# Optimization experiments

Hardware: AMD Instinct MI355X
Metric: run time of the kernel (lower is better)

The kernel has to match this reference:

```python
import jax, jax.numpy as jnp
import numpy as np

# Blade metric for Cl(1,3) inner product <~A B>_0: sign per basis blade =
# (-1)^{k(k-1)/2} * prod(eta_ii) with eta = diag(1,-1,-1,-1).
# Order: 1 | e0 e1 e2 e3 | e01 e02 e03 e12 e13 e23 | e012 e013 e023 e123 | e0123
BLADE_METRIC = jnp.array(
    [1.0,
     1.0, -1.0, -1.0, -1.0,
     1.0, 1.0, 1.0, -1.0, -1.0, -1.0,
     -1.0, -1.0, -1.0, 1.0,
     -1.0],
    dtype=jnp.float32,
)

B, H, N, MVC, SC = 8, 8, 1024, 8, 32


def setup_inputs() -> dict:
    key = jax.random.key(0)
    ks = jax.random.split(key, 6)
    mv_shape = (B, H, N, MVC, 16)
    s_shape = (B, H, N, SC)
    return {
        "q_mv": jax.random.normal(ks[0], mv_shape, dtype=jnp.float32),
        "k_mv": jax.random.normal(ks[1], mv_shape, dtype=jnp.float32),
        "v_mv": jax.random.normal(ks[2], mv_shape, dtype=jnp.float32),
        "q_s": jax.random.normal(ks[3], s_shape, dtype=jnp.float32),
        "k_s": jax.random.normal(ks[4], s_shape, dtype=jnp.float32),
        "v_s": jax.random.normal(ks[5], s_shape, dtype=jnp.float32),
    }


def reference(q_mv, k_mv, v_mv, q_s, k_s, v_s):
    *lead, n_out, mvc, _ = q_mv.shape
    n_in = k_mv.shape[-3]
    sc = q_s.shape[-1]
    d = 16 * mvc + sc  # total feature dim used for the softmax scale

    # Apply GA blade metric to queries, flatten mv channels, concat scalars.
    qf = jnp.concatenate(
        [(q_mv * BLADE_METRIC).reshape(*lead, n_out, mvc * 16), q_s], axis=-1
    )
    kf = jnp.concatenate([k_mv.reshape(*lead, n_in, mvc * 16), k_s], axis=-1)
    vf = jnp.concatenate([v_mv.reshape(*lead, n_in, mvc * 16), v_s], axis=-1)

    scores = jnp.einsum("bhid,bhjd->bhij", qf, kf) / jnp.sqrt(
        jnp.asarray(d, dtype=qf.dtype)
    )
    attn = jax.nn.softmax(scores, axis=-1)
    out = jnp.einsum("bhij,bhjd->bhid", attn, vf)

    out_mv = out[..., : mvc * 16].reshape(*lead, n_out, mvc, 16)
    out_s = out[..., mvc * 16 :]
    return out_mv, out_s
```

## Files before the change

kernel.cpp:

```cpp
#include <hip/hip_runtime.h>

typedef __attribute__((ext_vector_type(8))) _Float16 f16x8;
typedef __attribute__((ext_vector_type(4))) float f32x4;

#define BHn 64
#define Nn 1024

static constexpr int kOutMvElems = 8 * 8 * 1024 * 128;
static constexpr float kScaleLog2e = 0.11405506f;
static constexpr unsigned kNegMask = 0xBF1Cu;
static constexpr int kBlob = 20480;
static constexpr int kPair = 2 * kBlob;

typedef __attribute__((address_space(1))) const void* gas1_t;
typedef __attribute__((address_space(3))) void* las3_t;
__device__ __forceinline__ void dma16(const _Float16* g, _Float16* l) {
  __builtin_amdgcn_global_load_lds((gas1_t)g, (las3_t)l, 16, 0, 0);
}
__device__ __forceinline__ float fast_exp2(float x) {
  float r;
  asm("v_exp_f32 %0, %1" : "=v"(r) : "v"(x));
  return r;
}

__global__ __launch_bounds__(256) void pack_kernel(const float* __restrict__ kmv,
                                                   const float* __restrict__ ks,
                                                   const float* __restrict__ vmv,
                                                   const float* __restrict__ vs,
                                                   _Float16* __restrict__ KV) {
  __shared__ _Float16 tk[64][184];
  __shared__ _Float16 tv[160][72];
  const int kt = blockIdx.x;
  const int bh = blockIdx.y;
  const int tid = threadIdx.x;
#pragma unroll
  for (int i = 0; i < 5; ++i) {
    int s = tid + 256 * i;
    int key = s / 20, p = s - key * 20;
    int row = bh * Nn + kt * 64 + key;
    const float* src = (p < 16) ? (kmv + (size_t)row * 128 + p * 8)
                                : (ks + (size_t)row * 32 + (p - 16) * 8);
    float4 a = *(const float4*)src;
    float4 b = *(const float4*)(src + 4);
    f16x8 h;
    h[0] = (_Float16)a.x; h[1] = (_Float16)a.y; h[2] = (_Float16)a.z; h[3] = (_Float16)a.w;
    h[4] = (_Float16)b.x; h[5] = (_Float16)b.y; h[6] = (_Float16)b.z; h[7] = (_Float16)b.w;
    *(f16x8*)&tk[key][p * 8] = h;
  }
  for (int s = tid; s < 64 * 40; s += 256) {
    int key = s / 40, p = s - key * 40;
    int row = bh * Nn + kt * 64 + key;
    const float* src = (p < 32) ? (vmv + (size_t)row * 128 + p * 4)
                                : (vs + (size_t)row * 32 + (p - 32) * 4);
    float4 v = *(const float4*)src;
    int d = p * 4;
    tv[d + 0][key] = (_Float16)v.x;
    tv[d + 1][key] = (_Float16)v.y;
    tv[d + 2][key] = (_Float16)v.z;
    tv[d + 3][key] = (_Float16)v.w;
  }
  __syncthreads();
  _Float16* dst = KV + ((size_t)bh * 16 + kt) * kBlob;
#pragma unroll
  for (int i = 0; i < 5; ++i) {
    int u = tid + 256 * i;
    int p = u >> 6, key = u & 63;
    f16x8 h = *(const f16x8*)&tk[key][p * 8];
    *(f16x8*)&dst[p * 512 + key * 8] = h;
  }
#pragma unroll
  for (int i = 0; i < 5; ++i) {
    int u = tid + 256 * i;
    int s = u / 160, d = u - s * 160;
    int c32 = (s >> 2) * 32, gg = s & 3;
    f16x8 h;
#pragma unroll
    for (int i2 = 0; i2 < 8; ++i2) {
      int key = c32 + ((i2 < 4) ? (gg * 4 + i2) : (16 + gg * 4 + (i2 - 4)));
      h[i2] = tv[d][key];
    }
    *(f16x8*)&dst[10240 + u * 8] = h;
  }
}

__global__ __launch_bounds__(512, 1) void geo_attn_kernel(const float* __restrict__ qmv,
                                                          const float* __restrict__ qs,
                                                          const _Float16* __restrict__ KV,
                                                          float* __restrict__ out) {
  __shared__ __align__(16) _Float16 kv[2 * kPair];

  const int b = blockIdx.x;
  const int sw = (b & 7) * 32 + (b >> 3);
  const int qb = sw & 3;
  const int bh = sw >> 2;

  const int tid = threadIdx.x;
  const int w = tid >> 6;
  const int l = tid & 63;
  const int g = l >> 4;
  const int nn = l & 15;

  const _Float16* blob0 = KV + (size_t)bh * 16 * kBlob;

  int kbase[5];
#pragma unroll
  for (int c = 0; c < 5; ++c) kbase[c] = (4 * c + g) * 512 + nn * 8;
  int vbase[2];
#pragma unroll
  for (int ch = 0; ch < 2; ++ch) vbase[ch] = 10240 + (4 * ch + g) * 1280 + nn * 8;

  f16x8 qf[2][5];
#pragma unroll
  for (int q2 = 0; q2 < 2; ++q2) {
    const size_t qbase = (size_t)(bh * Nn + qb * 256 + w * 32 + q2 * 16 + nn);
#pragma unroll
    for (int c = 0; c < 5; ++c) {
      const float* src = (c < 4) ? (qmv + qbase * 128 + c * 32 + 8 * g)
                                 : (qs + qbase * 32 + 8 * g);
      float4 a = *(const float4*)src;
      float4 bb = *(const float4*)(src + 4);
      float x[8] = {a.x, a.y, a.z, a.w, bb.x, bb.y, bb.z, bb.w};
#pragma unroll
      for (int i = 0; i < 8; ++i) {
        float v = x[i] * kScaleLog2e;
        if (c < 4) {
          int idx = ((g & 1) << 3) + i;
          v = ((kNegMask >> idx) & 1u) ? -v : v;
        }
        qf[q2][c][i] = (_Float16)v;
      }
    }
  }

  f32x4 acc[2][10];
#pragma unroll
  for (int q2 = 0; q2 < 2; ++q2)
#pragma unroll
    for (int j = 0; j < 10; ++j) acc[q2][j] = (f32x4){0.f, 0.f, 0.f, 0.f};
  float Ma = 12.f, Mb = 12.f, La = 0.f, Lb = 0.f;

  f32x4 sa[4], sb[4];
  f16x8 paf[2], pbf[2];

  const int laneOff = l * 8 + w * 512;
  auto stage = [&](int t, int buf) {
    const _Float16* src = blob0 + (size_t)t * kPair + laneOff;
    _Float16* dst = &kv[buf * kPair + laneOff];
#pragma unroll
    for (int i = 0; i < 10; ++i) dma16(src + i * 4096, dst + i * 4096);
  };

  auto do_qk = [&](const _Float16* blob) {
#pragma unroll
    for (int kb = 0; kb < 4; ++kb) {
      sa[kb] = (f32x4){0.f, 0.f, 0.f, 0.f};
      sb[kb] = (f32x4){0.f, 0.f, 0.f, 0.f};
    }
    f16x8 kf[5][4];
#pragma unroll
    for (int c = 0; c < 2; ++c)
#pragma unroll
      for (int kb = 0; kb < 4; ++kb) kf[c][kb] = *(const f16x8*)&blob[kbase[c] + kb * 128];
#pragma unroll
    for (int c = 0; c < 5; ++c) {
      if (c + 2 < 5) {
#pragma unroll
        for (int kb = 0; kb < 4; ++kb)
          kf[c + 2][kb] = *(const f16x8*)&blob[kbase[c + 2] + kb * 128];
      }
#pragma unroll
      for (int kb = 0; kb < 4; ++kb) {
        sa[kb] = __builtin_amdgcn_mfma_f32_16x16x32_f16(kf[c][kb], qf[0][c], sa[kb], 0, 0, 0);
        sb[kb] = __builtin_amdgcn_mfma_f32_16x16x32_f16(kf[c][kb], qf[1][c], sb[kb], 0, 0, 0);
      }
    }
  };
  auto do_pv = [&](const _Float16* blob) {
    f16x8 vf[20];
#pragma unroll
    for (int i = 0; i < 4; ++i)
      vf[i] = *(const f16x8*)&blob[vbase[i / 10] + (i % 10) * 128];
#pragma unroll
    for (int i = 0; i < 20; ++i) {
      if (i + 4 < 20)
        vf[i + 4] = *(const f16x8*)&blob[vbase[(i + 4) / 10] + ((i + 4) % 10) * 128];
      const int ch = i / 10, j = i % 10;
      acc[0][j] = __builtin_amdgcn_mfma_f32_16x16x32_f16(paf[ch], vf[i], acc[0][j], 0, 0, 0);
      acc[1][j] = __builtin_amdgcn_mfma_f32_16x16x32_f16(pbf[ch], vf[i], acc[1][j], 0, 0, 0);
    }
  };
  auto do_softmax = [&]() {
    float rsa = 0.f, rsb = 0.f;
#pragma unroll
    for (int kb = 0; kb < 4; ++kb) {
      const int ch = kb >> 1, off = (kb & 1) * 4;
#pragma unroll
      for (int r = 0; r < 4; ++r) {
        float pa_ = fast_exp2(sa[kb][r] - Ma);
        float pb_ = fast_exp2(sb[kb][r] - Mb);
        rsa += pa_; rsb += pb_;
        paf[ch][off + r] = (_Float16)pa_;
        pbf[ch][off + r] = (_Float16)pb_;
      }
    }
    if (__builtin_expect(__any((int)(rsa > 3.2e4f || rsb > 3.2e4f)), 0)) {
      float lma = sa[0][0], lmb = sb[0][0];
#pragma unroll
      for (int kb = 0; kb < 4; ++kb)
#pragma unroll
        for (int r = 0; r < 4; ++r) {
          lma = fmaxf(lma, sa[kb][r]);
          lmb = fmaxf(lmb, sb[kb][r]);
        }
      lma = fmaxf(lma, __shfl_xor(lma, 16)); lma = fmaxf(lma, __shfl_xor(lma, 32));
      lmb = fmaxf(lmb, __shfl_xor(lmb, 16)); lmb = fmaxf(lmb, __shfl_xor(lmb, 32));
      float nMa = fmaxf(Ma, lma); float fsa = fast_exp2(Ma - nMa); Ma = nMa;
      float nMb = fmaxf(Mb, lmb); float fsb = fast_exp2(Mb - nMb); Mb = nMb;
      La *= fsa; Lb *= fsb;
      float fa[4], fb[4];
#pragma unroll
      for (int r = 0; r < 4; ++r) {
        fa[r] = __shfl(fsa, 4 * g + r, 16);
        fb[r] = __shfl(fsb, 4 * g + r, 16);
      }
#pragma unroll
      for (int j = 0; j < 10; ++j)
#pragma unroll
        for (int r = 0; r < 4; ++r) {
          acc[0][j][r] *= fa[r];
          acc[1][j][r] *= fb[r];
        }
      rsa = 0.f; rsb = 0.f;
#pragma unroll
      for (int kb = 0; kb < 4; ++kb) {
        const int ch = kb >> 1, off = (kb & 1) * 4;
#pragma unroll
        for (int r = 0; r < 4; ++r) {
          float pa_ = fast_exp2(sa[kb][r] - Ma);
          float pb_ = fast_exp2(sb[kb][r] - Mb);
          rsa += pa_; rsb += pb_;
          paf[ch][off + r] = (_Float16)pa_;
          pbf[ch][off + r] = (_Float16)pb_;
        }
      }
    }
    La += rsa;
    Lb += rsb;
  };

  stage(0, 0);
  __syncthreads();

  for (int t = 0; t < 8; ++t) {
    const int cur = t & 1;
    if (t < 7) stage(t + 1, cur ^ 1);
    const _Float16* base = &kv[cur * kPair];
#pragma unroll
    for (int h = 0; h < 2; ++h) {
      const _Float16* blob = base + h * kBlob;
      __builtin_amdgcn_s_setprio(1);
      do_qk(blob);
      __builtin_amdgcn_s_setprio(0);
      do_softmax();
      __builtin_amdgcn_s_setprio(1);
      do_pv(blob);
      __builtin_amdgcn_s_setprio(0);
    }
    __syncthreads();
  }

  La += __shfl_xor(La, 16); La += __shfl_xor(La, 32);
  Lb += __shfl_xor(Lb, 16); Lb += __shfl_xor(Lb, 32);
  float ria = 1.f / La, rib = 1.f / Lb;
  float ra[4], rb_[4];
#pragma unroll
  for (int r = 0; r < 4; ++r) {
    ra[r] = __shfl(ria, 4 * g + r, 16);
    rb_[r] = __shfl(rib, 4 * g + r, 16);
  }
  const int row0 = bh * Nn + qb * 256 + w * 32;
#pragma unroll
  for (int j = 0; j < 10; ++j) {
    const int d = 16 * j + nn;
#pragma unroll
    for (int r = 0; r < 4; ++r) {
      float v0 = acc[0][j][r] * ra[r];
      float v1 = acc[1][j][r] * rb_[r];
      const int r0 = row0 + 4 * g + r;
      const int r1 = row0 + 16 + 4 * g + r;
      if (d < 128) {
        out[(size_t)r0 * 128 + d] = v0;
        out[(size_t)r1 * 128 + d] = v1;
      } else {
        out[(size_t)kOutMvElems + (size_t)r0 * 32 + (d - 128)] = v0;
        out[(size_t)kOutMvElems + (size_t)r1 * 32 + (d - 128)] = v1;
      }
    }
  }
}

extern "C" void kernel_launch(void* const* d_in, const int* in_sizes, int n_in,
                              void* d_out, int out_size, void* d_ws, size_t ws_size,
                              hipStream_t stream) {
  const float* qmv = (const float*)d_in[0];
  const float* kmv = (const float*)d_in[1];
  const float* vmv = (const float*)d_in[2];
  const float* qs = (const float*)d_in[3];
  const float* ks = (const float*)d_in[4];
  const float* vs = (const float*)d_in[5];
  float* out = (float*)d_out;

  _Float16* KV = (_Float16*)d_ws;

  pack_kernel<<<dim3(16, BHn), dim3(256), 0, stream>>>(kmv, ks, vmv, vs, KV);
  geo_attn_kernel<<<dim3(256), dim3(512), 0, stream>>>(qmv, qs, KV, out);
}
```

Baseline: 76.78 us.

## Software-pipeline attention: overlap next tile's QK with previous tile's PV

Restructures the main loop so each step computes QK^T scores for the current K half-tile while doing the PV MFMAs for the previous half-tile, interleaving both MFMA chains and their LDS loads. Softmax of tile i then sits between clusters, and a final PV-only pass drains the pipeline. The aim is to hide softmax and LDS latency behind independent MFMA work. In exchange it needs more live registers for the interleaved K/V fragments and adds syncs per half-tile, and the buffer reuse timing (staging into the buffer whose V is still pending) must be correct.

```diff
diff --git a/kernel.cpp b/kernel.cpp
--- a/kernel.cpp
+++ b/kernel.cpp
@@ -150,43 +150,56 @@
     for (int i = 0; i < 10; ++i) dma16(src + i * 4096, dst + i * 4096);
   };
 
-  auto do_qk = [&](const _Float16* blob) {
+  auto cluster = [&](const _Float16* kblob, const _Float16* vblob, bool doPV) {
 #pragma unroll
     for (int kb = 0; kb < 4; ++kb) {
       sa[kb] = (f32x4){0.f, 0.f, 0.f, 0.f};
       sb[kb] = (f32x4){0.f, 0.f, 0.f, 0.f};
     }
     f16x8 kf[5][4];
-#pragma unroll
-    for (int c = 0; c < 2; ++c)
-#pragma unroll
-      for (int kb = 0; kb < 4; ++kb) kf[c][kb] = *(const f16x8*)&blob[kbase[c] + kb * 128];
+    f16x8 vf[20];
+#pragma unroll
+    for (int kb = 0; kb < 4; ++kb) kf[0][kb] = *(const f16x8*)&kblob[kbase[0] + kb * 128];
+    if (doPV) {
+#pragma unroll
+      for (int i = 0; i < 4; ++i)
+        vf[i] = *(const f16x8*)&vblob[vbase[i / 10] + (i % 10) * 128];
+    }
 #pragma unroll
     for (int c = 0; c < 5; ++c) {
-      if (c + 2 < 5) {
+      if (c + 1 < 5) {
 #pragma unroll
         for (int kb = 0; kb < 4; ++kb)
-          kf[c + 2][kb] = *(const f16x8*)&blob[kbase[c + 2] + kb * 128];
+          kf[c + 1][kb] = *(const f16x8*)&kblob[kbase[c + 1] + kb * 128];
       }
 #pragma unroll
       for (int kb = 0; kb < 4; ++kb) {
+        const int i = c * 4 + kb;
         sa[kb] = __builtin_amdgcn_mfma_f32_16x16x32_f16(kf[c][kb], qf[0][c], sa[kb], 0, 0, 0);
+        if (doPV && i + 4 < 20)
+          vf[i + 4] = *(const f16x8*)&vblob[vbase[(i + 4) / 10] + ((i + 4) % 10) * 128];
         sb[kb] = __builtin_amdgcn_mfma_f32_16x16x32_f16(kf[c][kb], qf[1][c], sb[kb], 0, 0, 0);
+        if (doPV) {
+          const int ch = i / 10, j = i % 10;
+          acc[0][j] = __builtin_amdgcn_mfma_f32_16x16x32_f16(paf[ch], vf[i], acc[0][j], 0, 0, 0);
+          acc[1][j] = __builtin_amdgcn_mfma_f32_16x16x32_f16(pbf[ch], vf[i], acc[1][j], 0, 0, 0);
+        }
       }
     }
   };
-  auto do_pv = [&](const _Float16* blob) {
-    f16x8 vf[20];
+  auto pv_only = [&](const _Float16* vblob) {
+    f16x8 vf[4];
 #pragma unroll
     for (int i = 0; i < 4; ++i)
-      vf[i] = *(const f16x8*)&blob[vbase[i / 10] + (i % 10) * 128];
+      vf[i & 3] = *(const f16x8*)&vblob[vbase[i / 10] + (i % 10) * 128];
 #pragma unroll
     for (int i = 0; i < 20; ++i) {
+      f16x8 cu = vf[i & 3];
       if (i + 4 < 20)
-        vf[i + 4] = *(const f16x8*)&blob[vbase[(i + 4) / 10] + ((i + 4) % 10) * 128];
+        vf[i & 3] = *(const f16x8*)&vblob[vbase[(i + 4) / 10] + ((i + 4) % 10) * 128];
       const int ch = i / 10, j = i % 10;
-      acc[0][j] = __builtin_amdgcn_mfma_f32_16x16x32_f16(paf[ch], vf[i], acc[0][j], 0, 0, 0);
-      acc[1][j] = __builtin_amdgcn_mfma_f32_16x16x32_f16(pbf[ch], vf[i], acc[1][j], 0, 0, 0);
+      acc[0][j] = __builtin_amdgcn_mfma_f32_16x16x32_f16(paf[ch], cu, acc[0][j], 0, 0, 0);
+      acc[1][j] = __builtin_amdgcn_mfma_f32_16x16x32_f16(pbf[ch], cu, acc[1][j], 0, 0, 0);
     }
   };
   auto do_softmax = [&]() {
@@ -251,23 +264,33 @@
   stage(0, 0);
   __syncthreads();
 
-  for (int t = 0; t < 8; ++t) {
-    const int cur = t & 1;
-    if (t < 7) stage(t + 1, cur ^ 1);
-    const _Float16* base = &kv[cur * kPair];
-#pragma unroll
-    for (int h = 0; h < 2; ++h) {
-      const _Float16* blob = base + h * kBlob;
-      __builtin_amdgcn_s_setprio(1);
-      do_qk(blob);
-      __builtin_amdgcn_s_setprio(0);
-      do_softmax();
-      __builtin_amdgcn_s_setprio(1);
-      do_pv(blob);
-      __builtin_amdgcn_s_setprio(0);
-    }
+  __builtin_amdgcn_s_setprio(1);
+  cluster(&kv[0], &kv[0], false);
+  __builtin_amdgcn_s_setprio(0);
+  do_softmax();
+  __syncthreads();
+  stage(1, 1);
+  __builtin_amdgcn_s_setprio(1);
+  cluster(&kv[kBlob], &kv[0], true);
+  __builtin_amdgcn_s_setprio(0);
+  do_softmax();
+  __syncthreads();
+
+  for (int t = 1; t < 8; ++t) {
+    const int c = t & 1;
+    __builtin_amdgcn_s_setprio(1);
+    cluster(&kv[c * kPair], &kv[(c ^ 1) * kPair + kBlob], true);
+    __builtin_amdgcn_s_setprio(0);
+    do_softmax();
     __syncthreads();
-  }
+    if (t < 7) stage(t + 1, c ^ 1);
+    __builtin_amdgcn_s_setprio(1);
+    cluster(&kv[c * kPair + kBlob], &kv[c * kPair], true);
+    __builtin_amdgcn_s_setprio(0);
+    do_softmax();
+    __syncthreads();
+  }
+  pv_only(&kv[kPair + kBlob]);
 
   La += __shfl_xor(La, 16); La += __shfl_xor(La, 32);
   Lb += __shfl_xor(Lb, 16); Lb += __shfl_xor(Lb, 32);
```

Result: slower. 78.75 us (+2.6%).

## Switch KV staging to triple-buffered per-blob pipeline with fine-grained vmcnt waits

Applied to the files above, without the earlier changes.

The double-buffered two-blob pipeline with a full __syncthreads per pair is replaced by a three-slot ring of single blobs. Each slot is prefetched two steps ahead, and the wait uses explicit s_waitcnt vmcnt plus a raw s_barrier, so DMA loads stay in flight across iterations. LDS use drops from 4 blobs to 3, and the V fragment prefetch buffer shrinks from 20 registers to a 4-entry ring to reduce register pressure. The hand-counted vmcnt depends on the stage issuing exactly five loads per lane; any other outstanding global load would break that assumption.

```diff
diff --git a/kernel.cpp b/kernel.cpp
--- a/kernel.cpp
+++ b/kernel.cpp
@@ -10,7 +10,6 @@
 static constexpr float kScaleLog2e = 0.11405506f;
 static constexpr unsigned kNegMask = 0xBF1Cu;
 static constexpr int kBlob = 20480;
-static constexpr int kPair = 2 * kBlob;
 
 typedef __attribute__((address_space(1))) const void* gas1_t;
 typedef __attribute__((address_space(3))) void* las3_t;
@@ -87,7 +86,7 @@
                                                           const float* __restrict__ qs,
                                                           const _Float16* __restrict__ KV,
                                                           float* __restrict__ out) {
-  __shared__ __align__(16) _Float16 kv[2 * kPair];
+  __shared__ __align__(16) _Float16 kv[3 * kBlob];
 
   const int b = blockIdx.x;
   const int sw = (b & 7) * 32 + (b >> 3);
@@ -144,10 +143,10 @@
 
   const int laneOff = l * 8 + w * 512;
   auto stage = [&](int t, int buf) {
-    const _Float16* src = blob0 + (size_t)t * kPair + laneOff;
-    _Float16* dst = &kv[buf * kPair + laneOff];
-#pragma unroll
-    for (int i = 0; i < 10; ++i) dma16(src + i * 4096, dst + i * 4096);
+    const _Float16* src = blob0 + (size_t)t * kBlob + laneOff;
+    _Float16* dst = &kv[buf * kBlob + w * 512];
+#pragma unroll
+    for (int i = 0; i < 5; ++i) dma16(src + i * 4096, dst + i * 4096);
   };
 
   auto do_qk = [&](const _Float16* blob) {
@@ -176,17 +175,18 @@
     }
   };
   auto do_pv = [&](const _Float16* blob) {
-    f16x8 vf[20];
+    f16x8 vf[4];
 #pragma unroll
     for (int i = 0; i < 4; ++i)
       vf[i] = *(const f16x8*)&blob[vbase[i / 10] + (i % 10) * 128];
 #pragma unroll
     for (int i = 0; i < 20; ++i) {
+      f16x8 cu = vf[i & 3];
       if (i + 4 < 20)
-        vf[i + 4] = *(const f16x8*)&blob[vbase[(i + 4) / 10] + ((i + 4) % 10) * 128];
+        vf[i & 3] = *(const f16x8*)&blob[vbase[(i + 4) / 10] + ((i + 4) % 10) * 128];
       const int ch = i / 10, j = i % 10;
-      acc[0][j] = __builtin_amdgcn_mfma_f32_16x16x32_f16(paf[ch], vf[i], acc[0][j], 0, 0, 0);
-      acc[1][j] = __builtin_amdgcn_mfma_f32_16x16x32_f16(pbf[ch], vf[i], acc[1][j], 0, 0, 0);
+      acc[0][j] = __builtin_amdgcn_mfma_f32_16x16x32_f16(paf[ch], cu, acc[0][j], 0, 0, 0);
+      acc[1][j] = __builtin_amdgcn_mfma_f32_16x16x32_f16(pbf[ch], cu, acc[1][j], 0, 0, 0);
     }
   };
   auto do_softmax = [&]() {
@@ -249,24 +249,22 @@
   };
 
   stage(0, 0);
-  __syncthreads();
-
-  for (int t = 0; t < 8; ++t) {
-    const int cur = t & 1;
-    if (t < 7) stage(t + 1, cur ^ 1);
-    const _Float16* base = &kv[cur * kPair];
-#pragma unroll
-    for (int h = 0; h < 2; ++h) {
-      const _Float16* blob = base + h * kBlob;
-      __builtin_amdgcn_s_setprio(1);
-      do_qk(blob);
-      __builtin_amdgcn_s_setprio(0);
-      do_softmax();
-      __builtin_amdgcn_s_setprio(1);
-      do_pv(blob);
-      __builtin_amdgcn_s_setprio(0);
-    }
-    __syncthreads();
+  stage(1, 1);
+
+  for (int t = 0; t < 16; ++t) {
+    if (t == 15) asm volatile("s_waitcnt vmcnt(0)" ::: "memory");
+    else         asm volatile("s_waitcnt vmcnt(5)" ::: "memory");
+    __builtin_amdgcn_s_barrier();
+    __builtin_amdgcn_sched_barrier(0);
+    if (t + 2 < 16) stage(t + 2, (t + 2) % 3);
+    const _Float16* blob = &kv[(t % 3) * kBlob];
+    __builtin_amdgcn_s_setprio(1);
+    do_qk(blob);
+    __builtin_amdgcn_s_setprio(0);
+    do_softmax();
+    __builtin_amdgcn_s_setprio(1);
+    do_pv(blob);
+    __builtin_amdgcn_s_setprio(0);
   }
 
   La += __shfl_xor(La, 16); La += __shfl_xor(La, 32);
```

Result: no change. 77.98 us (+1.6%).
